# Optimization experiments

Measured on AMD Instinct MI355X. Metric: run time of the kernel, lower is better.

The kernel has to match this reference:

```python
import jax, jax.numpy as jnp
import numpy as np

B, S, D = 2, 2048, 1024
H, HD = 16, 64
ROPE_BASE = 1000.0


def rope(x):
    # x: [B, H, S, hd]; interleaved (GPT-NeoX-style pairs) rotary embedding, base=1000
    d = x.shape[-1]
    theta = 1.0 / (ROPE_BASE ** (jnp.arange(0, d, 2, dtype=jnp.float32) / d))  # [d/2]
    theta = jnp.repeat(theta, 2)                                               # [d]
    pos = jnp.arange(x.shape[-2], dtype=jnp.float32)                           # [S]
    pm = pos[:, None] * theta[None, :]                                         # [S, d]
    cos, sin = jnp.cos(pm), jnp.sin(pm)
    # rotated: _x[..., 0::2] = -x[..., 1::2]; _x[..., 1::2] = x[..., 0::2]
    rot = jnp.stack([-x[..., 1::2], x[..., 0::2]], axis=-1).reshape(x.shape)
    return x * cos + rot * sin


def setup_inputs() -> dict:
    key = jax.random.key(0)
    ks = jax.random.split(key, 12)
    sc = 1.0 / np.sqrt(D)
    inp = {
        "query": jax.random.normal(ks[0], (B, S, D), jnp.float32),
        "key": jax.random.normal(ks[1], (B, S, D), jnp.float32),
        "value": jax.random.normal(ks[2], (B, S, D), jnp.float32),
        "mask": jnp.broadcast_to(jnp.tril(jnp.ones((S, S), jnp.int32)), (B, S, S)),
        "Wq": jax.random.normal(ks[3], (D, H * HD), jnp.float32) * sc,
        "bq": jax.random.normal(ks[4], (H * HD,), jnp.float32) * 0.01,
        "Wk": jax.random.normal(ks[5], (D, H * HD), jnp.float32) * sc,
        "bk": jax.random.normal(ks[6], (H * HD,), jnp.float32) * 0.01,
        "Wv": jax.random.normal(ks[7], (D, H * HD), jnp.float32) * sc,
        "bv": jax.random.normal(ks[8], (H * HD,), jnp.float32) * 0.01,
        "Wo": jax.random.normal(ks[9], (H * HD, D), jnp.float32) * sc,
        "bo": jax.random.normal(ks[10], (D,), jnp.float32) * 0.01,
    }
    return inp


def reference(query, key, value, mask, Wq, bq, Wk, bk, Wv, bv, Wo, bo):
    b = query.shape[0]
    split = lambda t: t.reshape(b, -1, H, HD).transpose(0, 2, 1, 3)  # [B,H,S,hd]
    q = split(query @ Wq + bq)
    k = split(key @ Wk + bk)
    v = split(value @ Wv + bv)
    qr, kr = rope(q), rope(k)
    scale = jnp.sqrt(jnp.float32(HD))
    num = jnp.exp(jnp.einsum("bhqd,bhkd->bhqk", qr, kr) / scale)           # [B,H,S,S]
    den = jnp.sum(jnp.exp(jnp.einsum("bhqd,bhkd->bhqk", q, k) / scale),
                  axis=-1, keepdims=True)                                   # [B,H,S,1]
    a = num / den
    a = jnp.where(mask[:, None, :, :] == 0, -jnp.inf, a)
    alpha = jax.nn.softmax(a, axis=-1)
    z = jnp.einsum("bhqk,bhkd->bhqd", alpha, v)
    z = z.transpose(0, 2, 1, 3).reshape(b, -1, H * HD)
    return z @ Wo + bo
```

## Files before the change

kernel.cpp:

```cpp
#include <hip/hip_runtime.h>


#define Bn 2
#define Sn 2048
#define Dn 1024
#define Hn 16
#define HDn 64

typedef __attribute__((ext_vector_type(8))) short bf16x8;
typedef __attribute__((ext_vector_type(8))) unsigned short u16x8;
typedef __attribute__((ext_vector_type(4))) unsigned short u16x4;
typedef __attribute__((ext_vector_type(4))) float f32x4;
typedef uint2 __attribute__((may_alias)) uint2a;

#define MFMA(a, b, c) __builtin_amdgcn_mfma_f32_16x16x32_bf16(a, b, c, 0, 0, 0)
#define Z4 ((f32x4){0.f, 0.f, 0.f, 0.f})

#define PRESC 0.18033688011112042f
#define C2 0.5287663729448977f

#define EXP2(x) __builtin_amdgcn_exp2f(x)
#define LOG2(x) __builtin_amdgcn_logf(x)

__device__ __forceinline__ unsigned short f2bf(float f) {
  unsigned int u = __builtin_bit_cast(unsigned int, f);
  u = (u + 0x7fffu + ((u >> 16) & 1u)) >> 16;
  return (unsigned short)u;
}
__device__ __forceinline__ float bf2f(unsigned short u) {
  return __builtin_bit_cast(float, (unsigned int)u << 16);
}

__device__ __forceinline__ unsigned int cvtpk(float lo, float hi) {
  unsigned int r;
  asm("v_cvt_pk_bf16_f32 %0, %1, %2" : "=v"(r) : "v"(lo), "v"(hi));
  return r;
}

__device__ __forceinline__ void gll16(const unsigned short* g, unsigned short* l) {
  __builtin_amdgcn_global_load_lds((const __attribute__((address_space(1))) void*)g,
                                   (__attribute__((address_space(3))) void*)l, 16, 0, 0);
}

#define FR(T, row, x) (*(const bf16x8*)&(T)[(row) * 64 + (((x) ^ ((row) & 7)) * 8)])

__global__ __launch_bounds__(256) void k_pre(
    const float* __restrict__ W0, const float* __restrict__ W1,
    const float* __restrict__ W2, const float* __restrict__ W3,
    unsigned short* __restrict__ O0, unsigned short* __restrict__ O1,
    unsigned short* __restrict__ O2, unsigned short* __restrict__ O3,
    const float* __restrict__ qa, const float* __restrict__ ka, const float* __restrict__ va,
    unsigned short* __restrict__ oq, unsigned short* __restrict__ ok,
    unsigned short* __restrict__ ov, float2* __restrict__ T) {
  __shared__ float t[64][65];
  const int b = blockIdx.x;
  const int tid = threadIdx.x;
  if (b < 256) {
    const int idx = b * 256 + tid;
    const int s = idx >> 5, i = idx & 31;
    const float theta = powf(1000.f, -(float)i / 32.f);
    const float pm = (float)s * theta;
    T[idx] = make_float2(cosf(pm), sinf(pm));
  } else if (b < 1280) {
    const int w = b - 256;
    const int which = w >> 8, rem = w & 255;
    const float* W = (which == 0) ? W0 : (which == 1) ? W1 : (which == 2) ? W2 : W3;
    unsigned short* O = (which == 0) ? O0 : (which == 1) ? O1 : (which == 2) ? O2 : O3;
    const int kb = (rem >> 4) * 64, nb = (rem & 15) * 64;
#pragma unroll
    for (int rep = 0; rep < 16; ++rep) {
      const int e = rep * 256 + tid;
      const int k = e >> 6, n = e & 63;
      t[k][n] = W[(kb + k) * Dn + nb + n];
    }
    __syncthreads();
#pragma unroll
    for (int rep = 0; rep < 16; ++rep) {
      const int e = rep * 256 + tid;
      const int n = e >> 6, k = e & 63;
      O[(nb + n) * Dn + kb + k] = f2bf(t[k][n]);
    }
  } else {
    const int c = b - 1280;
    const int z = c >> 11, cx = c & 2047;
    const float* s = (z == 0) ? qa : (z == 1) ? ka : va;
    unsigned short* d = (z == 0) ? oq : (z == 1) ? ok : ov;
    const size_t idx = ((size_t)cx * 256 + tid) * 8;
    float4 a0 = *(const float4*)(s + idx);
    float4 b0 = *(const float4*)(s + idx + 4);
    u16x8 pk;
    pk[0] = f2bf(a0.x); pk[1] = f2bf(a0.y); pk[2] = f2bf(a0.z); pk[3] = f2bf(a0.w);
    pk[4] = f2bf(b0.x); pk[5] = f2bf(b0.y); pk[6] = f2bf(b0.z); pk[7] = f2bf(b0.w);
    *(u16x8*)(d + idx) = pk;
  }
}

__global__ __launch_bounds__(256) void k_gemm_proj(
    const unsigned short* __restrict__ Qa, const unsigned short* __restrict__ Ka,
    const unsigned short* __restrict__ Va,
    const unsigned short* __restrict__ Wq, const unsigned short* __restrict__ Wk,
    const unsigned short* __restrict__ Wv,
    const float* __restrict__ bqp, const float* __restrict__ bkp, const float* __restrict__ bvp,
    const float2* __restrict__ trig,
    unsigned short* __restrict__ Qb, unsigned short* __restrict__ Kb,
    unsigned short* __restrict__ Qr, unsigned short* __restrict__ Kr,
    unsigned short* __restrict__ Vt) {
  __shared__ unsigned short SH[17408];
  unsigned short* Al = SH;
  unsigned short* Bl = SH + 8192;
  const int tid = threadIdx.x;
  const int wave = tid >> 6, lane = tid & 63, g = lane >> 4, li = lane & 15;
  const int mbase = blockIdx.x * 128, nbase = blockIdx.y * 128;
  const int wm = wave >> 1, wn = wave & 1;
  const int which = blockIdx.z;
  const unsigned short* A = (which == 0) ? Qa : (which == 1) ? Ka : Va;
  const unsigned short* Wt = (which == 0) ? Wq : (which == 1) ? Wk : Wv;
  const float* bias = (which == 0) ? bqp : (which == 1) ? bkp : bvp;

  f32x4 acc[4][4];
#pragma unroll
  for (int i = 0; i < 4; ++i)
#pragma unroll
    for (int j = 0; j < 4; ++j) acc[i][j] = Z4;

  float bv4[4];
#pragma unroll
  for (int nt = 0; nt < 4; ++nt) bv4[nt] = bias[nbase + wn * 64 + nt * 16 + li];

  const int lr8 = lane >> 3, lc = lane & 7;
  const int xc8 = (lc ^ lr8) * 8;
  const unsigned short* srcA = A + (size_t)(mbase + wave * 32 + lr8) * Dn + xc8;
  const unsigned short* srcB = Wt + (size_t)(nbase + wave * 32 + lr8) * Dn + xc8;

  for (int kb = 0; kb < Dn; kb += 64) {
    __syncthreads();
#pragma unroll
    for (int i = 0; i < 4; ++i) {
      gll16(srcA + kb + (size_t)i * (8 * Dn), &Al[(wave * 32 + i * 8) * 64]);
      gll16(srcB + kb + (size_t)i * (8 * Dn), &Bl[(wave * 32 + i * 8) * 64]);
    }
    __syncthreads();
#pragma unroll
    for (int kc = 0; kc < 2; ++kc) {
      bf16x8 af[4], bfr[4];
#pragma unroll
      for (int mt = 0; mt < 4; ++mt) af[mt] = FR(Al, wm * 64 + mt * 16 + li, kc * 4 + g);
#pragma unroll
      for (int nt = 0; nt < 4; ++nt) bfr[nt] = FR(Bl, wn * 64 + nt * 16 + li, kc * 4 + g);
#pragma unroll
      for (int mt = 0; mt < 4; ++mt)
#pragma unroll
        for (int nt = 0; nt < 4; ++nt)
          acc[mt][nt] = MFMA(af[mt], bfr[nt], acc[mt][nt]);
    }
  }

  if (which < 2) {
    unsigned short* Ob = (which == 0) ? Qb : Kb;
    unsigned short* Or = (which == 0) ? Qr : Kr;
    const float presc = (which == 0) ? PRESC : 1.f;
    __syncthreads();
#pragma unroll
    for (int mt = 0; mt < 4; ++mt)
#pragma unroll
      for (int nt = 0; nt < 4; ++nt) {
        const int nl = wn * 64 + nt * 16 + li;
#pragma unroll
        for (int r = 0; r < 4; ++r) {
          const int ml = wm * 64 + mt * 16 + 4 * g + r;
          SH[ml * 136 + nl] = f2bf((acc[mt][nt][r] + bv4[nt]) * presc);
        }
      }
    __syncthreads();
#pragma unroll
    for (int hp = 0; hp < 2; ++hp) {
#pragma unroll
      for (int pass = 0; pass < 4; ++pass) {
        const int row = pass * 32 + wave * 8 + (lane >> 3);
        const int nl = hp * 64 + (lane & 7) * 8;
        const int mg = mbase + row;
        const int bi = mg >> 11, sg = mg & (Sn - 1);
        const int ng = nbase + nl;
        const int h = ng >> 6, hd = ng & 63;
        const u16x8 v = *(const u16x8*)&SH[row * 136 + nl];
        u16x8 o;
        const float2* tp = trig + (sg << 5) + (hd >> 1);
#pragma unroll
        for (int j = 0; j < 4; ++j) {
          const float x0 = bf2f(v[2 * j]), x1 = bf2f(v[2 * j + 1]);
          const float2 cs = tp[j];
          o[2 * j] = f2bf(x0 * cs.x - x1 * cs.y);
          o[2 * j + 1] = f2bf(x1 * cs.x + x0 * cs.y);
        }
        const size_t oi = (((size_t)(bi * Hn + h)) * Sn + sg) * HDn + hd;
        *(u16x8*)(Ob + oi) = v;
        *(u16x8*)(Or + oi) = o;
      }
    }
  } else {
#pragma unroll
    for (int mt = 0; mt < 4; ++mt) {
#pragma unroll
      for (int nt = 0; nt < 4; ++nt) {
        const int n = nbase + wn * 64 + nt * 16 + li;
        const int h = n >> 6, hd = n & 63;
        const int m0 = mbase + wm * 64 + mt * 16 + 4 * g;
        const int b = m0 >> 11, s0 = m0 & (Sn - 1);
        u16x4 pk;
#pragma unroll
        for (int r = 0; r < 4; ++r) pk[r] = f2bf(acc[mt][nt][r] + bv4[nt]);
        *(u16x4*)&Vt[(((size_t)(b * Hn + h)) * HDn + hd) * Sn + s0] = pk;
      }
    }
  }
}

__global__ __launch_bounds__(256) void k_gemm_out(const unsigned short* __restrict__ A,
                                                  const unsigned short* __restrict__ Wt,
                                                  const float* __restrict__ bias,
                                                  float* __restrict__ out) {
  __shared__ unsigned short Al[64 * 64];
  __shared__ unsigned short Bl[128 * 64];
  const int tid = threadIdx.x;
  const int wave = tid >> 6, lane = tid & 63, g = lane >> 4, li = lane & 15;
  const int mbase = blockIdx.x * 64, nbase = blockIdx.y * 128;
  const int wm = wave >> 1, wn = wave & 1;

  f32x4 acc[2][4];
#pragma unroll
  for (int i = 0; i < 2; ++i)
#pragma unroll
    for (int j = 0; j < 4; ++j) acc[i][j] = Z4;

  float bv4[4];
#pragma unroll
  for (int nt = 0; nt < 4; ++nt) bv4[nt] = bias[nbase + wn * 64 + nt * 16 + li];

  const int lr8 = lane >> 3, lc = lane & 7;
  const int xc8 = (lc ^ lr8) * 8;
  const unsigned short* srcA = A + (size_t)(mbase + wave * 16 + lr8) * Dn + xc8;
  const unsigned short* srcB = Wt + (size_t)(nbase + wave * 32 + lr8) * Dn + xc8;

  for (int kb = 0; kb < Dn; kb += 64) {
    __syncthreads();
#pragma unroll
    for (int i = 0; i < 2; ++i)
      gll16(srcA + kb + (size_t)i * (8 * Dn), &Al[(wave * 16 + i * 8) * 64]);
#pragma unroll
    for (int i = 0; i < 4; ++i)
      gll16(srcB + kb + (size_t)i * (8 * Dn), &Bl[(wave * 32 + i * 8) * 64]);
    __syncthreads();
#pragma unroll
    for (int kc = 0; kc < 2; ++kc) {
      bf16x8 af[2], bfr[4];
#pragma unroll
      for (int mt = 0; mt < 2; ++mt) af[mt] = FR(Al, wm * 32 + mt * 16 + li, kc * 4 + g);
#pragma unroll
      for (int nt = 0; nt < 4; ++nt) bfr[nt] = FR(Bl, wn * 64 + nt * 16 + li, kc * 4 + g);
#pragma unroll
      for (int mt = 0; mt < 2; ++mt)
#pragma unroll
        for (int nt = 0; nt < 4; ++nt)
          acc[mt][nt] = MFMA(af[mt], bfr[nt], acc[mt][nt]);
    }
  }

#pragma unroll
  for (int mt = 0; mt < 2; ++mt)
#pragma unroll
    for (int nt = 0; nt < 4; ++nt) {
      const int n = nbase + wn * 64 + nt * 16 + li;
#pragma unroll
      for (int r = 0; r < 4; ++r) {
        const int m = mbase + wm * 32 + mt * 16 + 4 * g + r;
        out[(size_t)m * Dn + n] = acc[mt][nt][r] + bv4[nt];
      }
    }
}

__global__ __launch_bounds__(256, 4) void k_attn(
    const unsigned short* __restrict__ Qr, const unsigned short* __restrict__ Kr,
    const unsigned short* __restrict__ Qb, const unsigned short* __restrict__ Kb,
    const unsigned short* __restrict__ Vt, unsigned short* __restrict__ Zb) {
  __shared__ unsigned short KT[2][8192];
  __shared__ unsigned short Pl[4][1024];

  const int tid = threadIdx.x;
  const int wave = tid >> 6, lane = tid & 63, g = lane >> 4, li = lane & 15;
  const int bid = blockIdx.x;
  const int x = bid & 7, m = bid >> 3;
  const int Qd = m >> 5, wv = m & 31, v = wv & 7;
  const int bh = x * 4 + (wv >> 3);
  const int qt = (Qd == 0) ? v : (Qd == 1) ? 15 - v : (Qd == 2) ? 16 + v : 31 - v;
  const int qw = qt * 64 + wave * 16;
  const size_t kvbase = (size_t)bh * (Sn * HDn);

  bf16x8 qrf[2], qbf[2];
#pragma unroll
  for (int kc = 0; kc < 2; ++kc) {
    const size_t a = kvbase + (size_t)(qw + li) * HDn + kc * 32 + g * 8;
    qrf[kc] = *(const bf16x8*)(Qr + a);
    qbf[kc] = *(const bf16x8*)(Qb + a);
  }

  const int lr8 = lane >> 3, lc = lane & 7;
  const int xc8 = (lc ^ lr8) * 8;

  const unsigned short* srcPA = Kb + kvbase + (size_t)(wave * 32 + lr8) * HDn + xc8;
  const int tw = wave >> 1, rbB = (wave & 1) * 32;
  const unsigned short* srcKrB = Kr + kvbase + (size_t)(rbB + lr8) * HDn + xc8;
  const unsigned short* srcVtB = Vt + kvbase + (size_t)(rbB + lr8) * Sn + xc8;
  const size_t strIB = tw ? (size_t)(8 * Sn) : (size_t)(8 * HDn);
  unsigned short* myP = &Pl[wave][0];

  bool dm[4];
#pragma unroll
  for (int r = 0; r < 4; ++r) dm[r] = (4 * g + r) <= li;

#define STAGE_PA(kb_, buf_)                                 \
  do {                                                      \
    unsigned short* d_ = &KT[buf_][(wave * 32) * 64];       \
    const unsigned short* s_ = srcPA + (size_t)(kb_)*HDn;   \
    gll16(s_, d_);                                          \
    gll16(s_ + 8 * HDn, d_ + 8 * 64);                       \
    gll16(s_ + 16 * HDn, d_ + 16 * 64);                     \
    gll16(s_ + 24 * HDn, d_ + 24 * 64);                     \
  } while (0)

#define STAGE_B(kb_, buf_)                                                    \
  do {                                                                        \
    unsigned short* d_ = &KT[buf_][tw * 4096 + rbB * 64];                     \
    const unsigned short* s_ =                                                \
        tw ? (srcVtB + (size_t)(kb_)) : (srcKrB + (size_t)(kb_)*HDn);         \
    gll16(s_, d_);                                                            \
    gll16(s_ + strIB, d_ + 8 * 64);                                           \
    gll16(s_ + 2 * strIB, d_ + 16 * 64);                                      \
    gll16(s_ + 3 * strIB, d_ + 24 * 64);                                      \
  } while (0)

  float d4[4] = {0.f, 0.f, 0.f, 0.f};
  STAGE_PA(0, 0);
  __syncthreads();
  for (int t = 0; t < Sn / 128; ++t) {
    if (t + 1 < Sn / 128) STAGE_PA((t + 1) * 128, (t + 1) & 1);
    const unsigned short* TK = &KT[t & 1][0];
#pragma unroll
    for (int nt = 0; nt < 8; ++nt) {
      const int krow = nt * 16 + li;
      const bf16x8 kf0 = FR(TK, krow, g), kf1 = FR(TK, krow, 4 + g);
      f32x4 s = Z4;
      s = MFMA(kf0, qbf[0], s);
      s = MFMA(kf1, qbf[1], s);
#pragma unroll
      for (int r = 0; r < 4; ++r) d4[r] += EXP2(s[r]);
    }
    __syncthreads();
  }
  float den = (d4[0] + d4[1]) + (d4[2] + d4[3]);
  den += __shfl_xor(den, 16);
  den += __shfl_xor(den, 32);
  const float Lc = LOG2(den) - C2;
  const f32x4 mLc = {-Lc, -Lc, -Lc, -Lc};

  f32x4 accz[4];
#pragma unroll
  for (int i = 0; i < 4; ++i) accz[i] = Z4;
  float ws[4] = {0.f, 0.f, 0.f, 0.f};
  const int NTB = qt + 1;

  STAGE_B(0, 0);
  __syncthreads();
  for (int t = 0; t < NTB; ++t) {
    if (t + 1 < NTB) STAGE_B((t + 1) * 64, (t + 1) & 1);
    const unsigned short* T0 = &KT[t & 1][0];
    const unsigned short* TV = &KT[t & 1][0] + 4096;
    const bool last = (t == qt);
#pragma unroll
    for (int nt = 0; nt < 4; ++nt) {
      float w4[4];
      if (!last || nt <= wave) {
        const int krow = nt * 16 + li;
        const bf16x8 kf0 = FR(T0, krow, g), kf1 = FR(T0, krow, 4 + g);
        f32x4 s = mLc;
        s = MFMA(kf0, qrf[0], s);
        s = MFMA(kf1, qrf[1], s);
        if (last && nt == wave) {
#pragma unroll
          for (int r = 0; r < 4; ++r) {
            const float e = EXP2(EXP2(s[r]));
            w4[r] = dm[r] ? e : 0.f;
            ws[r] += w4[r];
          }
        } else {
#pragma unroll
          for (int r = 0; r < 4; ++r) {
            w4[r] = EXP2(EXP2(s[r]));
            ws[r] += w4[r];
          }
        }
      } else {
        w4[0] = w4[1] = w4[2] = w4[3] = 0.f;
      }
      const int adr = li * 64 + (((nt * 2 + (g >> 1)) ^ (li & 7)) * 8) + (g & 1) * 4;
      *(uint2a*)&myP[adr] = (uint2a){cvtpk(w4[0], w4[1]), cvtpk(w4[2], w4[3])};
    }
    __builtin_amdgcn_sched_barrier(0);
#pragma unroll
    for (int kc = 0; kc < 2; ++kc) {
      const bf16x8 pa = FR(myP, li, kc * 4 + g);
#pragma unroll
      for (int n2 = 0; n2 < 4; ++n2) {
        const bf16x8 vb = FR(TV, n2 * 16 + li, kc * 4 + g);
        accz[n2] = MFMA(pa, vb, accz[n2]);
      }
    }
    __syncthreads();
  }

  float wsum = (ws[0] + ws[1]) + (ws[2] + ws[3]);
  wsum += __shfl_xor(wsum, 16);
  wsum += __shfl_xor(wsum, 32);
  float rw[4];
#pragma unroll
  for (int r = 0; r < 4; ++r) rw[r] = 1.f / __shfl(wsum, 4 * g + r);
  const int b = bh >> 4, h = bh & 15;
#pragma unroll
  for (int n2 = 0; n2 < 4; ++n2) {
#pragma unroll
    for (int r = 0; r < 4; ++r) {
      const int hd = n2 * 16 + li;
      const int q = qw + 4 * g + r;
      Zb[((size_t)(b * Sn + q)) * Dn + h * HDn + hd] = f2bf(accz[n2][r] * rw[r]);
    }
  }
#undef STAGE_PA
#undef STAGE_B
}

extern "C" void kernel_launch(void* const* d_in, const int* in_sizes, int n_in,
                              void* d_out, int out_size, void* d_ws, size_t ws_size,
                              hipStream_t stream) {
  const float* query = (const float*)d_in[0];
  const float* key   = (const float*)d_in[1];
  const float* value = (const float*)d_in[2];
  const float* Wq = (const float*)d_in[4];
  const float* bq = (const float*)d_in[5];
  const float* Wk = (const float*)d_in[6];
  const float* bk = (const float*)d_in[7];
  const float* Wv = (const float*)d_in[8];
  const float* bv = (const float*)d_in[9];
  const float* Wo = (const float*)d_in[10];
  const float* bo = (const float*)d_in[11];

  char* ws = (char*)d_ws;
  const size_t MB = 1ull << 20;
  unsigned short* Wqt = (unsigned short*)(ws + 0 * MB);
  unsigned short* Wkt = (unsigned short*)(ws + 2 * MB);
  unsigned short* Wvt = (unsigned short*)(ws + 4 * MB);
  unsigned short* Wot = (unsigned short*)(ws + 6 * MB);
  float2* trig        = (float2*)(ws + 8 * MB);
  unsigned short* Qa  = (unsigned short*)(ws + 9 * MB);
  unsigned short* Ka  = (unsigned short*)(ws + 17 * MB);
  unsigned short* Va  = (unsigned short*)(ws + 25 * MB);
  unsigned short* Qb  = (unsigned short*)(ws + 33 * MB);
  unsigned short* Kb  = (unsigned short*)(ws + 41 * MB);
  unsigned short* Qr  = (unsigned short*)(ws + 49 * MB);
  unsigned short* Kr  = (unsigned short*)(ws + 57 * MB);
  unsigned short* Vt  = (unsigned short*)(ws + 65 * MB);
  unsigned short* Zb  = (unsigned short*)(ws + 73 * MB);

  k_pre<<<7424, 256, 0, stream>>>(Wq, Wk, Wv, Wo, Wqt, Wkt, Wvt, Wot,
                                  query, key, value, Qa, Ka, Va, trig);
  k_gemm_proj<<<dim3(32, 8, 3), 256, 0, stream>>>(Qa, Ka, Va, Wqt, Wkt, Wvt,
                                                  bq, bk, bv, trig, Qb, Kb, Qr, Kr, Vt);
  k_attn<<<1024, 256, 0, stream>>>(Qr, Kr, Qb, Kb, Vt, Zb);
  k_gemm_out<<<dim3(64, 8), 256, 0, stream>>>(Zb, Wot, bo, (float*)d_out);
}
```

Baseline: 135.4 us.

## Split denominator pass by key rows per wave and reduce across waves in LDS

```diff
diff --git a/kernel.cpp b/kernel.cpp
--- a/kernel.cpp
+++ b/kernel.cpp
@@ -12,6 +12,7 @@
 typedef __attribute__((ext_vector_type(4))) unsigned short u16x4;
 typedef __attribute__((ext_vector_type(4))) float f32x4;
 typedef uint2 __attribute__((may_alias)) uint2a;
+typedef float __attribute__((may_alias)) floata;
 
 #define MFMA(a, b, c) __builtin_amdgcn_mfma_f32_16x16x32_bf16(a, b, c, 0, 0, 0)
 #define Z4 ((f32x4){0.f, 0.f, 0.f, 0.f})
@@ -292,19 +293,20 @@
   const int Qd = m >> 5, wv = m & 31, v = wv & 7;
   const int bh = x * 4 + (wv >> 3);
   const int qt = (Qd == 0) ? v : (Qd == 1) ? 15 - v : (Qd == 2) ? 16 + v : 31 - v;
-  const int qw = qt * 64 + wave * 16;
+  const int q0 = qt * 64;
+  const int qw = q0 + wave * 16;
   const size_t kvbase = (size_t)bh * (Sn * HDn);
-
-  bf16x8 qrf[2], qbf[2];
-#pragma unroll
-  for (int kc = 0; kc < 2; ++kc) {
-    const size_t a = kvbase + (size_t)(qw + li) * HDn + kc * 32 + g * 8;
-    qrf[kc] = *(const bf16x8*)(Qr + a);
-    qbf[kc] = *(const bf16x8*)(Qb + a);
-  }
 
   const int lr8 = lane >> 3, lc = lane & 7;
   const int xc8 = (lc ^ lr8) * 8;
+
+  bf16x8 qbfA[4][2];
+#pragma unroll
+  for (int jq = 0; jq < 4; ++jq)
+#pragma unroll
+    for (int kc = 0; kc < 2; ++kc)
+      qbfA[jq][kc] =
+          *(const bf16x8*)(Qb + kvbase + (size_t)(q0 + jq * 16 + li) * HDn + kc * 32 + g * 8);
 
   const unsigned short* srcPA = Kb + kvbase + (size_t)(wave * 32 + lr8) * HDn + xc8;
   const int tw = wave >> 1, rbB = (wave & 1) * 32;
@@ -338,29 +340,53 @@
     gll16(s_ + 3 * strIB, d_ + 24 * 64);                                      \
   } while (0)
 
-  float d4[4] = {0.f, 0.f, 0.f, 0.f};
+  float dacc[4][4];
+#pragma unroll
+  for (int jq = 0; jq < 4; ++jq)
+#pragma unroll
+    for (int r = 0; r < 4; ++r) dacc[jq][r] = 0.f;
+
   STAGE_PA(0, 0);
   __syncthreads();
   for (int t = 0; t < Sn / 128; ++t) {
     if (t + 1 < Sn / 128) STAGE_PA((t + 1) * 128, (t + 1) & 1);
     const unsigned short* TK = &KT[t & 1][0];
 #pragma unroll
-    for (int nt = 0; nt < 8; ++nt) {
-      const int krow = nt * 16 + li;
+    for (int sub = 0; sub < 2; ++sub) {
+      const int krow = wave * 32 + sub * 16 + li;
       const bf16x8 kf0 = FR(TK, krow, g), kf1 = FR(TK, krow, 4 + g);
-      f32x4 s = Z4;
-      s = MFMA(kf0, qbf[0], s);
-      s = MFMA(kf1, qbf[1], s);
-#pragma unroll
-      for (int r = 0; r < 4; ++r) d4[r] += EXP2(s[r]);
-    }
-    __syncthreads();
-  }
-  float den = (d4[0] + d4[1]) + (d4[2] + d4[3]);
-  den += __shfl_xor(den, 16);
-  den += __shfl_xor(den, 32);
+      f32x4 s[4];
+#pragma unroll
+      for (int jq = 0; jq < 4; ++jq) {
+        s[jq] = MFMA(kf0, qbfA[jq][0], Z4);
+        s[jq] = MFMA(kf1, qbfA[jq][1], s[jq]);
+      }
+#pragma unroll
+      for (int jq = 0; jq < 4; ++jq)
+#pragma unroll
+        for (int r = 0; r < 4; ++r) dacc[jq][r] += EXP2(s[jq][r]);
+    }
+    __syncthreads();
+  }
+
+  floata* Dred = (floata*)&Pl[0][0];
+#pragma unroll
+  for (int jq = 0; jq < 4; ++jq) {
+    float pd = (dacc[jq][0] + dacc[jq][1]) + (dacc[jq][2] + dacc[jq][3]);
+    pd += __shfl_xor(pd, 16);
+    pd += __shfl_xor(pd, 32);
+    if (lane < 16) Dred[wave * 64 + jq * 16 + li] = pd;
+  }
+  __syncthreads();
+  const float den = (Dred[0 * 64 + wave * 16 + li] + Dred[1 * 64 + wave * 16 + li]) +
+                    (Dred[2 * 64 + wave * 16 + li] + Dred[3 * 64 + wave * 16 + li]);
   const float Lc = LOG2(den) - C2;
   const f32x4 mLc = {-Lc, -Lc, -Lc, -Lc};
+
+  bf16x8 qrf[2];
+#pragma unroll
+  for (int kc = 0; kc < 2; ++kc)
+    qrf[kc] = *(const bf16x8*)(Qr + kvbase + (size_t)(qw + li) * HDn + kc * 32 + g * 8);
 
   f32x4 accz[4];
 #pragma unroll
```

Measured after the change: 135.2 us, median of 2. About the same (-0.2%).
